# Kernel optimization log

Measured on AMD Instinct MI355X. Metric: run time of the kernel, lower is better.

## Reference

```python
import jax, jax.numpy as jnp
from jax import lax
import numpy as np

PRE_NMS_TOPN = 2000
POST_NMS_TOPN = 300
NMS_IOU_THRESHOLD = 0.7
EPS = 1e-8


def setup_inputs() -> dict:
    key = jax.random.key(0)
    k1, k2 = jax.random.split(key, 2)
    B, H, W, A = 64, 100, 100, 9
    # small-magnitude deltas so exp(dh/dw) stays sane, as real RPN outputs do
    rpn_bbox_deltas = jax.random.normal(k1, (B, H, W, A * 4), dtype=jnp.float32) * 0.1
    rpn_labels = jax.random.uniform(k2, (B, H, W, A), dtype=jnp.float32)
    # grid anchors, normalized coords, 3 scales x 3 ratios = 9 per position
    ys = (jnp.arange(H, dtype=jnp.float32) + 0.5) / H
    xs = (jnp.arange(W, dtype=jnp.float32) + 0.5) / W
    scales = jnp.array([0.1, 0.2, 0.4], dtype=jnp.float32)
    ratios = jnp.array([0.5, 1.0, 2.0], dtype=jnp.float32)
    hh = (scales[:, None] * jnp.sqrt(ratios)[None, :]).reshape(-1)  # [9]
    ww = (scales[:, None] / jnp.sqrt(ratios)[None, :]).reshape(-1)  # [9]
    cy, cx = jnp.meshgrid(ys, xs, indexing="ij")  # [H,W]
    cy, cx = cy[..., None], cx[..., None]         # [H,W,1]
    anchors = jnp.stack(
        [cy - hh / 2, cx - ww / 2, cy + hh / 2, cx + ww / 2], axis=-1
    ).reshape(-1, 4)  # [H*W*9, 4] = [90000, 4]
    return {"rpn_bbox_deltas": rpn_bbox_deltas, "rpn_labels": rpn_labels, "anchors": anchors}


def _decode_deltas(anchors, deltas):
    # anchors [N,4] (y1,x1,y2,x2), deltas [B,N,4] (dy,dx,dh,dw)
    anc_h = anchors[:, 2] - anchors[:, 0]
    anc_w = anchors[:, 3] - anchors[:, 1]
    anc_cy = anchors[:, 0] + 0.5 * anc_h
    anc_cx = anchors[:, 1] + 0.5 * anc_w
    h = jnp.exp(deltas[..., 2]) * anc_h
    w = jnp.exp(deltas[..., 3]) * anc_w
    cy = deltas[..., 0] * anc_h + anc_cy
    cx = deltas[..., 1] * anc_w + anc_cx
    y1 = cy - 0.5 * h
    x1 = cx - 0.5 * w
    return jnp.stack([y1, x1, y1 + h, x1 + w], axis=-1)  # [B,N,4]


def _nms_single(boxes):
    # boxes [PRE,4] already sorted by score descending; greedy hard NMS
    n = boxes.shape[0]
    area = jnp.maximum(boxes[:, 2] - boxes[:, 0], 0.0) * jnp.maximum(boxes[:, 3] - boxes[:, 1], 0.0)
    idx = jnp.arange(n)

    def body(i, keep):
        b = boxes[i]
        yy1 = jnp.maximum(b[0], boxes[:, 0])
        xx1 = jnp.maximum(b[1], boxes[:, 1])
        yy2 = jnp.minimum(b[2], boxes[:, 2])
        xx2 = jnp.minimum(b[3], boxes[:, 3])
        inter = jnp.maximum(yy2 - yy1, 0.0) * jnp.maximum(xx2 - xx1, 0.0)
        iou = inter / (area[i] + area - inter + EPS)
        suppress = (iou > NMS_IOU_THRESHOLD) & (idx > i) & keep[i]
        return keep & ~suppress

    keep = lax.fori_loop(0, n, body, jnp.ones((n,), dtype=bool))
    # compact kept boxes (score order) into fixed [POST,4], zero-padded
    pos = jnp.where(keep, jnp.cumsum(keep) - 1, POST_NMS_TOPN)
    pos = jnp.minimum(pos, POST_NMS_TOPN)
    out = jnp.zeros((POST_NMS_TOPN + 1, 4), dtype=boxes.dtype).at[pos].set(boxes)[:POST_NMS_TOPN]
    return jnp.clip(out, 0.0, 1.0)  # clip_boxes=True in tf combined NMS


def reference(rpn_bbox_deltas, rpn_labels, anchors):
    B = rpn_bbox_deltas.shape[0]
    N = anchors.shape[0]
    deltas = rpn_bbox_deltas.reshape(B, N, 4)
    labels = rpn_labels.reshape(B, N)
    boxes = _decode_deltas(anchors, deltas)             # [B,N,4]
    _, pre_idx = lax.top_k(labels, PRE_NMS_TOPN)        # [B,PRE] sorted desc
    pre_boxes = jnp.take_along_axis(boxes, pre_idx[..., None], axis=1)  # [B,PRE,4]
    roi_bboxes = jax.vmap(_nms_single)(pre_boxes)       # [B,POST,4]
    return lax.stop_gradient(roi_bboxes)
```

## Files before the change

### kernel.cpp

```cpp
#include <hip/hip_runtime.h>
#include <stdint.h>


#define PRE 2000
#define POST 300
#define TILE 512
#define IOU_THR 0.7f
#define EPSV 1e-8f
#define SORTN 2048
#define NBINS 2048
#define DESTCAP 4096
#define CANDCAP 512
#define CONS 1984
#define SL 16
#define KBUF 768

typedef unsigned long long u64;

__device__ __forceinline__ uint32_t flip_f32(uint32_t b) {
    return b ^ ((uint32_t)((int32_t)b >> 31) | 0x80000000u);
}

__device__ __forceinline__ int bin_of(float s) {
    int bn = (int)(s * 2048.0f);
    return min(max(bn, 0), NBINS - 1);
}

__device__ __forceinline__ u64 make_key(float s, int idx, int bn) {
    uint32_t ub = flip_f32(__float_as_uint(s));
    return ((u64)ub << 32) | ((uint32_t)bn << 20) |
           (uint32_t)(0xFFFFF - idx);
}

__device__ __forceinline__ bool iou_gt(const float4& bi, float ai,
                                       const float4& bj, float aj) {
    float yy1 = fmaxf(bi.x, bj.x);
    float xx1 = fmaxf(bi.y, bj.y);
    float yy2 = fminf(bi.z, bj.z);
    float xx2 = fminf(bi.w, bj.w);
    float inter = fmaxf(yy2 - yy1, 0.f) * fmaxf(xx2 - xx1, 0.f);
    float iou = inter / (ai + aj - inter + EPSV);
    return iou > IOU_THR;
}

__device__ __forceinline__ float area_of(const float4& bx) {
    return fmaxf(bx.z - bx.x, 0.f) * fmaxf(bx.w - bx.y, 0.f);
}

__device__ __forceinline__ float4 decode_key(u64 key, const float4* dl,
                                             const float4* anchors, int N) {
    uint32_t idx = 0xFFFFFu - (uint32_t)(key & 0xFFFFFull);
    if (idx >= (uint32_t)N) return make_float4(0.f, 0.f, 0.f, 0.f);
    float4 d  = dl[idx];
    float4 an = anchors[idx];
    float ah  = an.z - an.x;
    float aw  = an.w - an.y;
    float acy = an.x + 0.5f * ah;
    float acx = an.y + 0.5f * aw;
    float h   = expf(d.z) * ah;
    float w   = expf(d.w) * aw;
    float cy  = d.x * ah + acy;
    float cx  = d.y * aw + acx;
    float y1  = cy - 0.5f * h;
    float x1  = cx - 0.5f * w;
    return make_float4(y1, x1, y1 + h, x1 + w);
}

__device__ __forceinline__ u64 cs_keep(u64 v, u64 pv, int i, int j, int k) {
    bool lower   = ((i & j) == 0);
    bool desc    = ((i & k) == 0);
    bool keepmax = (desc == lower);
    u64 mx = v > pv ? v : pv;
    u64 mn = v > pv ? pv : v;
    return keepmax ? mx : mn;
}

__global__ __launch_bounds__(256) void k1_gather(
    const float4* __restrict__ score4,
    u64* __restrict__ g_pairs,
    int* __restrict__ g_scnt,
    uint32_t* __restrict__ g_shist,
    int N)
{
    const int blk = blockIdx.x;
    const int b   = blk / SL;
    const int s   = blk % SL;
    const int tid = threadIdx.x;
    const int lane = tid & 63;
    const int F4PB = N >> 2;
    const int F4PS = (F4PB + SL - 1) / SL;

    __shared__ u64 keybuf[KBUF];
    __shared__ u64 binbuf[KBUF];
    __shared__ uint32_t hist64[64];
    __shared__ int base64[64];
    __shared__ uint32_t cur64[64];
    __shared__ int kcnt;

    if (tid < 64) { hist64[tid] = 0u; cur64[tid] = 0u; }
    if (tid == 0) kcnt = 0;
    __syncthreads();

    const float4* src = score4 + (size_t)b * F4PB;
    const int n0 = s * F4PS, n1 = min(n0 + F4PS, F4PB);
    for (int n = n0 + tid; n < n1; n += 256) {
        float4 v = src[n];
        float sv[4] = {v.x, v.y, v.z, v.w};
#pragma unroll
        for (int c = 0; c < 4; ++c) {
            int bn = bin_of(sv[c]);
            if (bn >= CONS) {
                int q = atomicAdd(&kcnt, 1);
                if (q < KBUF) keybuf[q] = make_key(sv[c], 4 * n + c, bn);
            }
        }
    }
    __syncthreads();

    const int raw = kcnt;
    const int lc  = min(raw, KBUF);

    for (int i = tid; i < lc; i += 256) {
        int b64 = (int)((keybuf[i] >> 20) & 0xFFFu) - CONS;
        atomicAdd(&hist64[b64], 1u);
    }
    __syncthreads();

    if (tid < 64) {
        int h = (int)hist64[lane];
        int ssum = h;
#pragma unroll
        for (int off = 1; off < 64; off <<= 1) {
            int t = __shfl_down(ssum, off, 64);
            if (lane + off < 64) ssum += t;
        }
        base64[lane] = ssum - h;
    }
    __syncthreads();

    for (int i = tid; i < lc; i += 256) {
        u64 key = keybuf[i];
        int b64 = (int)((key >> 20) & 0xFFFu) - CONS;
        int p = (int)atomicAdd(&cur64[b64], 1u);
        binbuf[base64[b64] + p] = key;
    }
    __syncthreads();

    if (tid == 0) g_scnt[b * SL + s] = raw;
    if (tid < 64) g_shist[((size_t)b * SL + s) * 64 + tid] = hist64[tid];
    u64* gp = g_pairs + ((size_t)b * SL + s) * KBUF;
    for (int i = tid; i < lc; i += 256) gp[i] = binbuf[i];
}

__global__ __launch_bounds__(1024) void k2_sort(
    const float4* __restrict__ score4,
    const u64*  __restrict__ g_pairs,
    const int*  __restrict__ g_scnt,
    const uint32_t* __restrict__ g_shist,
    u64* __restrict__ g_sorted,
    int N)
{
    const int b    = blockIdx.x;
    const int tid  = threadIdx.x;
    const int lane = tid & 63;
    const int wv   = tid >> 6;

    __shared__ u64 dest[DESTCAP];
    __shared__ uint32_t hist2048[NBINS];
    __shared__ u64 cand[CANDCAP];
    __shared__ uint32_t shist[SL][64];
    __shared__ int srcb[SL][64];
    __shared__ int sbase[SL][64];
    __shared__ int tot64[64];
    __shared__ int segbase64[64];
    __shared__ uint32_t wtot[16];
    __shared__ int sh_flag, sh_total, sh_bsel, sh_tprime, sh_cnt, sh_nc;
    __shared__ uint32_t sh_pivot;

    const int F4PB = N >> 2;

    shist[tid >> 6][tid & 63] = g_shist[(size_t)b * SL * 64 + tid];
    if (tid == 0) {
        int f = 0;
#pragma unroll
        for (int s = 0; s < SL; ++s)
            if (g_scnt[b * SL + s] > KBUF) f = 1;
        sh_flag = f;
    }
    __syncthreads();

    if (tid < 64) {
        int acc = 0;
#pragma unroll
        for (int s = 0; s < SL; ++s) acc += (int)shist[s][tid];
        tot64[tid] = acc;
        if (acc > 128) sh_flag = 1;
    }
    {
        int h = (int)shist[wv][lane];
        int ssum = h;
#pragma unroll
        for (int off = 1; off < 64; off <<= 1) {
            int t = __shfl_down(ssum, off, 64);
            if (lane + off < 64) ssum += t;
        }
        srcb[wv][lane] = ssum - h;
    }
    __syncthreads();

    if (tid < 64) {
        int t0 = tot64[lane];
        int ssum = t0;
#pragma unroll
        for (int off = 1; off < 64; off <<= 1) {
            int t = __shfl_down(ssum, off, 64);
            if (lane + off < 64) ssum += t;
        }
        segbase64[lane] = ssum - t0;
        if (lane == 0) sh_total = ssum;
    }
    __syncthreads();
    const int total = sh_total;
    if (tid == 0 && (total < PRE || total > DESTCAP)) sh_flag = 1;
    {
        int s   = tid >> 6;
        int b64 = tid & 63;
        int pre = 0;
        for (int s2 = 0; s2 < s; ++s2) pre += (int)shist[s2][b64];
        sbase[s][b64] = segbase64[b64] + pre;
    }
    __syncthreads();
    const bool flag = (sh_flag != 0);

    if (!flag) {
        const int cs = min(g_scnt[b * SL + wv], KBUF);
        const u64* gp = g_pairs + ((size_t)b * SL + wv) * KBUF;
        for (int i = lane; i < cs; i += 64) {
            u64 key = gp[i];
            int b64 = (int)((key >> 20) & 0xFFFu) - CONS;
            dest[sbase[wv][b64] + (i - srcb[wv][b64])] = key;
        }
        __syncthreads();
        for (int sgi = wv; sgi < 64; sgi += 16) {
            int n = tot64[sgi];
            if (n <= 0) continue;
            int base = segbase64[sgi];
            if (n <= 64) {
                u64 e = (lane < n) ? dest[base + lane] : 0ull;
#pragma unroll
                for (int k = 2; k <= 64; k <<= 1)
                    for (int j = k >> 1; j > 0; j >>= 1)
                        e = cs_keep(e, __shfl_xor(e, j, 64), lane, j, k);
                if (lane < n) dest[base + lane] = e;
            } else {
                u64 e0 = (lane < n) ? dest[base + lane] : 0ull;
                u64 e1 = (lane + 64 < n) ? dest[base + lane + 64] : 0ull;
#pragma unroll
                for (int k = 2; k <= 128; k <<= 1) {
                    for (int j = k >> 1; j > 0; j >>= 1) {
                        if (j == 64) {
                            u64 a = e0, c = e1;
                            e0 = cs_keep(a, c, lane, 64, k);
                            e1 = cs_keep(c, a, lane + 64, 64, k);
                        } else {
                            e0 = cs_keep(e0, __shfl_xor(e0, j, 64), lane, j, k);
                            e1 = cs_keep(e1, __shfl_xor(e1, j, 64), lane + 64, j, k);
                        }
                    }
                }
                if (lane < n) dest[base + lane] = e0;
                if (lane + 64 < n) dest[base + lane + 64] = e1;
            }
        }
        __syncthreads();
        g_sorted[(size_t)b * SORTN + tid]        = dest[tid];
        g_sorted[(size_t)b * SORTN + tid + 1024] = dest[tid + 1024];
    } else {
        hist2048[tid] = 0u; hist2048[tid + 1024] = 0u;
        if (tid == 0) { sh_cnt = 0; sh_nc = 0; }
        __syncthreads();
        const float4* src = score4 + (size_t)b * F4PB;
        for (int n = tid; n < F4PB; n += 1024) {
            float4 v = src[n];
            atomicAdd(&hist2048[bin_of(v.x)], 1u);
            atomicAdd(&hist2048[bin_of(v.y)], 1u);
            atomicAdd(&hist2048[bin_of(v.z)], 1u);
            atomicAdd(&hist2048[bin_of(v.w)], 1u);
        }
        __syncthreads();
        {
            const int i0 = wv * 128 + lane;
            const int i1 = i0 + 64;
            int h0 = (int)hist2048[i0];
            int h1 = (int)hist2048[i1];
            int s0 = h0, s1 = h1;
#pragma unroll
            for (int off = 1; off < 64; off <<= 1) {
                int t0 = __shfl_down(s0, off, 64);
                int t1 = __shfl_down(s1, off, 64);
                if (lane + off < 64) { s0 += t0; s1 += t1; }
            }
            int sum_h1 = __shfl(s1, 0, 64);
            if (lane == 0) wtot[wv] = (uint32_t)(__shfl(s0, 0, 64) + sum_h1);
            __syncthreads();
            int offtot = 0;
            for (int w2 = wv + 1; w2 < 16; ++w2) offtot += (int)wtot[w2];
            int S0 = s0 + sum_h1 + offtot;
            int S1 = s1 + offtot;
            if (S0 >= PRE && S0 - h0 < PRE) { sh_bsel = i0; sh_tprime = PRE - (S0 - h0); }
            if (S1 >= PRE && S1 - h1 < PRE) { sh_bsel = i1; sh_tprime = PRE - (S1 - h1); }
        }
        __syncthreads();
        const int bsel   = sh_bsel;
        const int tprime = sh_tprime;
        for (int n = tid; n < F4PB; n += 1024) {
            float4 v = src[n];
            float sv[4] = {v.x, v.y, v.z, v.w};
#pragma unroll
            for (int c = 0; c < 4; ++c) {
                int bn = bin_of(sv[c]);
                if (bn >= bsel) {
                    u64 key = make_key(sv[c], 4 * n + c, bn);
                    if (bn > bsel) {
                        int q = atomicAdd(&sh_cnt, 1);
                        if (q < SORTN) dest[q] = key;
                    } else {
                        int t = atomicAdd(&sh_nc, 1);
                        if (t < CANDCAP) cand[t] = key;
                    }
                }
            }
        }
        __syncthreads();
        const int nc = min(sh_nc, CANDCAP);
        for (int i = tid; i < nc; i += 1024) {
            uint32_t vi = (uint32_t)(cand[i] >> 32);
            int g = 0, e = 0;
            for (int j = 0; j < nc; ++j) {
                uint32_t vj = (uint32_t)(cand[j] >> 32);
                g += (vj > vi);
                e += (vj == vi);
            }
            if (g < tprime && g + e >= tprime) sh_pivot = vi;
        }
        __syncthreads();
        const uint32_t pivot = sh_pivot;
        for (int i = tid; i < nc; i += 1024) {
            uint32_t vi = (uint32_t)(cand[i] >> 32);
            if (vi >= pivot) {
                int q = atomicAdd(&sh_cnt, 1);
                if (q < SORTN) dest[q] = cand[i];
            }
        }
        __syncthreads();
        const int tt = min(sh_cnt, SORTN);
        for (int q = tt + tid; q < SORTN; q += 1024) dest[q] = 0ull;
        __syncthreads();
        {
            const int i0 = wv * 128 + lane;
            const int i1 = i0 + 64;
            u64 e0 = dest[i0];
            u64 e1 = dest[i1];
            for (int k = 2; k <= SORTN; k <<= 1) {
                for (int j = k >> 1; j > 0; j >>= 1) {
                    if (j >= 128) {
                        dest[i0] = e0;
                        dest[i1] = e1;
                        __syncthreads();
                        u64 p0 = dest[i0 ^ j];
                        u64 p1 = dest[i1 ^ j];
                        __syncthreads();
                        e0 = cs_keep(e0, p0, i0, j, k);
                        e1 = cs_keep(e1, p1, i1, j, k);
                    } else if (j == 64) {
                        u64 a = e0, c = e1;
                        e0 = cs_keep(a, c, i0, 64, k);
                        e1 = cs_keep(c, a, i1, 64, k);
                    } else {
                        e0 = cs_keep(e0, __shfl_xor(e0, j, 64), i0, j, k);
                        e1 = cs_keep(e1, __shfl_xor(e1, j, 64), i1, j, k);
                    }
                }
            }
            g_sorted[(size_t)b * SORTN + i0] = e0;
            g_sorted[(size_t)b * SORTN + i1] = e1;
        }
    }
}

__global__ __launch_bounds__(256) void k4_supmat(
    const float4* __restrict__ deltas,
    const float4* __restrict__ anchors,
    const u64*  __restrict__ g_sorted,
    float4* __restrict__ g_boxes,
    uint32_t* __restrict__ g_supmat,
    uint32_t* __restrict__ g_supT,
    int N)
{
    const int b   = blockIdx.x >> 4;
    const int s   = blockIdx.x & 15;
    const int tid = threadIdx.x;

    __shared__ float4 box[TILE];

    const float4* dl = deltas + (size_t)b * N;
#pragma unroll
    for (int k = 0; k < 2; ++k) {
        int r = tid + k * 256;
        box[r] = decode_key(g_sorted[(size_t)b * SORTN + r], dl, anchors, N);
    }
    __syncthreads();

    if (s == 0) {
#pragma unroll
        for (int k = 0; k < 2; ++k) {
            int r = tid + k * 256;
            g_boxes[(size_t)b * TILE + r] = box[r];
        }
    }

    const int rbase = s * 32;
#pragma unroll
    for (int k = 0; k < 2; ++k) {
        int idx = tid + k * 256;
        int row = rbase + (idx & 31);
        int w   = idx >> 5;
        int jbase = w << 5;
        float4 bi = box[row];
        float  ai = area_of(bi);
        uint32_t bits = 0u;
        if (jbase + 31 > row) {
#pragma unroll
            for (int c = 0; c < 32; ++c) {
                int j = jbase + c;
                float4 bj = box[j];
                float  aj = area_of(bj);
                bool gt = (j > row) & iou_gt(bi, ai, bj, aj);
                bits |= ((uint32_t)gt) << c;
            }
        }
        g_supmat[((size_t)b * TILE + row) * 16 + w] = bits;
    }

    if (s < 8 && tid < 128) {
        int q  = s;
        int j  = tid >> 1;
        int w2 = tid & 1;
        int C  = q * 64 + j;
        float4 bc = box[C];
        float  ac = area_of(bc);
        uint32_t bits = 0u;
#pragma unroll
        for (int c = 0; c < 32; ++c) {
            int R = q * 64 + w2 * 32 + c;
            float4 br = box[R];
            float  ar = area_of(br);
            bool gt = (R < C) & iou_gt(br, ar, bc, ac);
            bits |= ((uint32_t)gt) << c;
        }
        g_supT[((size_t)b * TILE + C) * 2 + w2] = bits;
    }
}

__global__ __launch_bounds__(64) void k5_sweep(
    const uint32_t* __restrict__ g_supmat,
    const u64*    __restrict__ g_supT64,
    const u64*    __restrict__ g_sorted,
    const float4* __restrict__ deltas,
    const float4* __restrict__ anchors,
    const float4* __restrict__ g_boxes,
    float4* __restrict__ out,
    int N)
{
    const int b    = blockIdx.x;
    const int lane = threadIdx.x;

    __shared__ uint32_t kept[POST];
    __shared__ u64 sh_keepbits[TILE / 64];
    __shared__ int sh_kc;
    __shared__ float4 fbox[PRE];
    __shared__ float  farea[PRE];
    __shared__ uint32_t fmask[(PRE - TILE + 31) / 32];

    const u64* tdbase = g_supT64 + (size_t)b * TILE;

    uint32_t removedw = 0u;
    int kc = 0, nq = 0;
    u64 cw_cur = tdbase[lane];
    for (int q = 0; q < TILE / 64; ++q) {
        u64 cw_next = (q < TILE / 64 - 1) ? tdbase[(q + 1) * 64 + lane] : 0ull;
        const int cbase = q << 6;
        uint32_t rlo = (uint32_t)__builtin_amdgcn_readlane((int)removedw, 2 * q);
        uint32_t rhi = (uint32_t)__builtin_amdgcn_readlane((int)removedw, 2 * q + 1);
        u64 avail = ~(((u64)rhi << 32) | rlo);
        u64 K = 0ull;
        while (avail) {
            int i = __ffsll((long long)avail) - 1;
            K |= (1ull << i);
            u64 supp = __ballot(((cw_cur >> i) & 1ull) != 0ull);
            avail &= ~(supp | (1ull << i));
        }
        if (lane == 0) sh_keepbits[q] = K;
        kc += __popcll(K);
        nq = q + 1;
        if (kc >= POST) break;
        if (K) {
            const int w = lane & 15;
            const int g = lane >> 4;
            const uint32_t* gs =
                g_supmat + ((size_t)b * TILE + cbase + g * 16) * 16 + w;
            uint32_t acc = 0u;
#pragma unroll
            for (int r = 0; r < 16; ++r) {
                uint32_t v = gs[(size_t)r * 16];
                uint32_t m = (uint32_t)0 - (uint32_t)((K >> (g * 16 + r)) & 1ull);
                acc |= (v & m);
            }
            acc |= (uint32_t)__shfl_xor((int)acc, 16, 64);
            acc |= (uint32_t)__shfl_xor((int)acc, 32, 64);
            if (lane < 16) removedw |= acc;
        }
        cw_cur = cw_next;
    }
    {
        int base = 0;
        for (int q = 0; q < nq; ++q) {
            u64 kbq = sh_keepbits[q];
            int pos = base + __popcll(kbq & ((1ull << lane) - 1));
            if (((kbq >> lane) & 1ull) && pos < POST)
                kept[pos] = (uint32_t)(q * 64 + lane);
            base += __popcll(kbq);
        }
        if (lane == 0) sh_kc = min(kc, POST);
    }
    __syncthreads();
    int kcf = sh_kc;
    const bool fellback = (kcf < POST);

    if (fellback) {
        const float4* dl = deltas + (size_t)b * N;
        for (int r = lane; r < PRE; r += 64) {
            float4 bx = decode_key(g_sorted[(size_t)b * SORTN + r], dl,
                                   anchors, N);
            fbox[r]  = bx;
            farea[r] = area_of(bx);
        }
        for (int w = lane; w < (PRE - TILE + 31) / 32; w += 64) fmask[w] = 0u;
        __syncthreads();
        for (int j = TILE + lane; j < PRE; j += 64) {
            float4 bj = fbox[j];
            float  aj = farea[j];
            bool supd = false;
            for (int k = 0; k < kcf; ++k) {
                int i = (int)kept[k];
                if (iou_gt(fbox[i], farea[i], bj, aj)) { supd = true; break; }
            }
            if (supd) atomicOr(&fmask[(j - TILE) >> 5], 1u << ((j - TILE) & 31));
        }
        __syncthreads();
        int i = TILE;
        while (i < PRE && kcf < POST) {
            while (i < PRE && ((fmask[(i - TILE) >> 5] >> ((i - TILE) & 31)) & 1u)) ++i;
            if (i >= PRE) break;
            if (lane == 0) kept[kcf] = (uint32_t)i;
            ++kcf;
            if (kcf >= POST) break;
            float4 bi = fbox[i];
            float  ai = farea[i];
            for (int j = i + 1 + lane; j < PRE; j += 64) {
                if (iou_gt(bi, ai, fbox[j], farea[j]))
                    atomicOr(&fmask[(j - TILE) >> 5], 1u << ((j - TILE) & 31));
            }
            ++i;
            __syncthreads();
        }
    }
    __syncthreads();

    float4* ob = out + (size_t)b * POST;
    for (int r = lane; r < POST; r += 64) {
        float4 o = make_float4(0.f, 0.f, 0.f, 0.f);
        if (r < kcf) {
            int ki = (int)kept[r];
            float4 bx = fellback ? fbox[ki]
                                 : g_boxes[(size_t)b * TILE + ki];
            o.x = fminf(fmaxf(bx.x, 0.f), 1.f);
            o.y = fminf(fmaxf(bx.y, 0.f), 1.f);
            o.z = fminf(fmaxf(bx.z, 0.f), 1.f);
            o.w = fminf(fmaxf(bx.w, 0.f), 1.f);
        }
        ob[r] = o;
    }
}

extern "C" void kernel_launch(void* const* d_in, const int* in_sizes, int n_in,
                              void* d_out, int out_size, void* d_ws, size_t ws_size,
                              hipStream_t stream) {
    const float4* deltas  = (const float4*)d_in[0];
    const float*  labels  = (const float*)d_in[1];
    const float4* anchors = (const float4*)d_in[2];
    const float4* score4  = (const float4*)labels;
    float4*       outp    = (float4*)d_out;
    const int N = in_sizes[2] / 4;
    const int B = in_sizes[1] / N;

    char* ws = (char*)d_ws;
    const size_t SZ_BOXES  = (size_t)B * TILE * 16;
    const size_t SZ_PAIRS  = (size_t)B * SL * KBUF * 8;
    const size_t SZ_SORTED = (size_t)B * SORTN * 8;
    const size_t SZ_SUPMAT = (size_t)B * TILE * 16 * 4;
    const size_t SZ_SUPT   = (size_t)B * TILE * 8;
    const size_t SZ_SHIST  = (size_t)B * SL * 64 * 4;
    float4*   g_boxes  = (float4*)ws;
    u64*      g_pairs  = (u64*)(ws + SZ_BOXES);
    u64*      g_sorted = (u64*)(ws + SZ_BOXES + SZ_PAIRS);
    uint32_t* g_supmat = (uint32_t*)(ws + SZ_BOXES + SZ_PAIRS + SZ_SORTED);
    uint32_t* g_supT   = (uint32_t*)(ws + SZ_BOXES + SZ_PAIRS + SZ_SORTED + SZ_SUPMAT);
    uint32_t* g_shist  = (uint32_t*)(ws + SZ_BOXES + SZ_PAIRS + SZ_SORTED + SZ_SUPMAT + SZ_SUPT);
    int*      g_scnt   = (int*)((char*)g_shist + SZ_SHIST);

    k1_gather<<<B * SL, 256, 0, stream>>>(score4, g_pairs, g_scnt, g_shist, N);
    k2_sort<<<B, 1024, 0, stream>>>(score4, g_pairs, g_scnt, g_shist,
                                    g_sorted, N);
    k4_supmat<<<B * 16, 256, 0, stream>>>(deltas, anchors, g_sorted,
                                          g_boxes, g_supmat, g_supT, N);
    k5_sweep<<<B, 64, 0, stream>>>(g_supmat, (const u64*)g_supT, g_sorted,
                                   deltas, anchors, g_boxes, outp, N);
}
```

Measured before the change: 75.68 us.

## Fuse four NMS pipeline kernels into one cooperative mega-kernel with grid syncs

Replaces the four separate launches (gather, sort, suppression matrix, sweep) with one cooperative kernel that runs each phase in turn, separated by grid-wide syncs, and shares a union of LDS layouts. This removes launch gaps and the drain between kernels. The sort phase is reworked for 256-thread blocks: the slice count is halved with a larger per-slice buffer, the prefix-scan offsets are recomputed, and the fallback bitonic sort runs as strided loops. A fallback path keeps four 256-thread kernels for when the cooperative launch cannot fit. The risks are the cost of grid.sync, the narrower sort phase (1024 threads down to 256), and host-side occupancy queries made on every call.

After: 101.5 us. 34.1% more time.

```diff
diff --git a/kernel.cpp b/kernel.cpp
--- a/kernel.cpp
+++ b/kernel.cpp
@@ -1,4 +1,5 @@
 #include <hip/hip_runtime.h>
+#include <hip/hip_cooperative_groups.h>
 #include <stdint.h>
 
 
@@ -9,13 +10,14 @@
 #define EPSV 1e-8f
 #define SORTN 2048
 #define NBINS 2048
-#define DESTCAP 4096
+#define DESTCAP 3584
 #define CANDCAP 512
 #define CONS 1984
-#define SL 16
-#define KBUF 768
+#define SL 8
+#define KBUF 1536
 
 typedef unsigned long long u64;
+namespace cg = cooperative_groups;
 
 __device__ __forceinline__ uint32_t flip_f32(uint32_t b) {
     return b ^ ((uint32_t)((int32_t)b >> 31) | 0x80000000u);
@@ -75,30 +77,43 @@
     return keepmax ? mx : mn;
 }
 
-__global__ __launch_bounds__(256) void k1_gather(
-    const float4* __restrict__ score4,
-    u64* __restrict__ g_pairs,
-    int* __restrict__ g_scnt,
-    uint32_t* __restrict__ g_shist,
-    int N)
-{
-    const int blk = blockIdx.x;
-    const int b   = blk / SL;
-    const int s   = blk % SL;
-    const int tid = threadIdx.x;
+struct P1L {
+    u64 keybuf[KBUF];
+    u64 binbuf[KBUF];
+    uint32_t hist64[64];
+    int base64[64];
+    uint32_t cur64[64];
+    int kcnt;
+};
+struct P2L {
+    u64 dest[DESTCAP];
+    int off[SL][64];
+    int tot64[64];
+    int segbase64[64];
+    int flag, total, bsel, tprime, cnt, nc;
+    uint32_t pivot;
+};
+struct P3L { float4 box[TILE]; };
+struct P4L {
+    uint32_t kept[POST];
+    u64 keepbits[TILE / 64];
+    uint32_t fmask[(PRE - TILE + 31) / 32];
+};
+union MegaLDS { P1L p1; P2L p2; P3L p3; P4L p4; };
+
+__device__ void phase1(MegaLDS& u, int blk, int tid,
+                       const float4* __restrict__ score4,
+                       u64* __restrict__ g_pairs, int* __restrict__ g_scnt,
+                       uint32_t* __restrict__ g_shist, int N)
+{
+    const int b = blk / SL;
+    const int s = blk % SL;
     const int lane = tid & 63;
     const int F4PB = N >> 2;
     const int F4PS = (F4PB + SL - 1) / SL;
 
-    __shared__ u64 keybuf[KBUF];
-    __shared__ u64 binbuf[KBUF];
-    __shared__ uint32_t hist64[64];
-    __shared__ int base64[64];
-    __shared__ uint32_t cur64[64];
-    __shared__ int kcnt;
-
-    if (tid < 64) { hist64[tid] = 0u; cur64[tid] = 0u; }
-    if (tid == 0) kcnt = 0;
+    if (tid < 64) { u.p1.hist64[tid] = 0u; u.p1.cur64[tid] = 0u; }
+    if (tid == 0) u.p1.kcnt = 0;
     __syncthreads();
 
     const float4* src = score4 + (size_t)b * F4PB;
@@ -110,151 +125,127 @@
         for (int c = 0; c < 4; ++c) {
             int bn = bin_of(sv[c]);
             if (bn >= CONS) {
-                int q = atomicAdd(&kcnt, 1);
-                if (q < KBUF) keybuf[q] = make_key(sv[c], 4 * n + c, bn);
-            }
-        }
-    }
-    __syncthreads();
-
-    const int raw = kcnt;
+                int q = atomicAdd(&u.p1.kcnt, 1);
+                if (q < KBUF) u.p1.keybuf[q] = make_key(sv[c], 4 * n + c, bn);
+            }
+        }
+    }
+    __syncthreads();
+
+    const int raw = u.p1.kcnt;
     const int lc  = min(raw, KBUF);
 
     for (int i = tid; i < lc; i += 256) {
-        int b64 = (int)((keybuf[i] >> 20) & 0xFFFu) - CONS;
-        atomicAdd(&hist64[b64], 1u);
+        int b64 = (int)((u.p1.keybuf[i] >> 20) & 0xFFFu) - CONS;
+        atomicAdd(&u.p1.hist64[b64], 1u);
     }
     __syncthreads();
 
     if (tid < 64) {
-        int h = (int)hist64[lane];
+        int h = (int)u.p1.hist64[lane];
         int ssum = h;
 #pragma unroll
         for (int off = 1; off < 64; off <<= 1) {
             int t = __shfl_down(ssum, off, 64);
             if (lane + off < 64) ssum += t;
         }
-        base64[lane] = ssum - h;
+        u.p1.base64[lane] = ssum - h;
     }
     __syncthreads();
 
     for (int i = tid; i < lc; i += 256) {
-        u64 key = keybuf[i];
+        u64 key = u.p1.keybuf[i];
         int b64 = (int)((key >> 20) & 0xFFFu) - CONS;
-        int p = (int)atomicAdd(&cur64[b64], 1u);
-        binbuf[base64[b64] + p] = key;
+        int p = (int)atomicAdd(&u.p1.cur64[b64], 1u);
+        u.p1.binbuf[u.p1.base64[b64] + p] = key;
     }
     __syncthreads();
 
     if (tid == 0) g_scnt[b * SL + s] = raw;
-    if (tid < 64) g_shist[((size_t)b * SL + s) * 64 + tid] = hist64[tid];
+    if (tid < 64) g_shist[((size_t)b * SL + s) * 64 + tid] = u.p1.hist64[tid];
     u64* gp = g_pairs + ((size_t)b * SL + s) * KBUF;
-    for (int i = tid; i < lc; i += 256) gp[i] = binbuf[i];
-}
-
-__global__ __launch_bounds__(1024) void k2_sort(
-    const float4* __restrict__ score4,
-    const u64*  __restrict__ g_pairs,
-    const int*  __restrict__ g_scnt,
-    const uint32_t* __restrict__ g_shist,
-    u64* __restrict__ g_sorted,
-    int N)
-{
-    const int b    = blockIdx.x;
-    const int tid  = threadIdx.x;
+    for (int i = tid; i < lc; i += 256) gp[i] = u.p1.binbuf[i];
+}
+
+__device__ void phase2(MegaLDS& u, int b, int tid,
+                       const float4* __restrict__ score4,
+                       const u64* __restrict__ g_pairs,
+                       const int* __restrict__ g_scnt,
+                       const uint32_t* __restrict__ g_shist,
+                       u64* __restrict__ g_sorted, int N)
+{
     const int lane = tid & 63;
-    const int wv   = tid >> 6;
-
-    __shared__ u64 dest[DESTCAP];
-    __shared__ uint32_t hist2048[NBINS];
-    __shared__ u64 cand[CANDCAP];
-    __shared__ uint32_t shist[SL][64];
-    __shared__ int srcb[SL][64];
-    __shared__ int sbase[SL][64];
-    __shared__ int tot64[64];
-    __shared__ int segbase64[64];
-    __shared__ uint32_t wtot[16];
-    __shared__ int sh_flag, sh_total, sh_bsel, sh_tprime, sh_cnt, sh_nc;
-    __shared__ uint32_t sh_pivot;
-
+    const int wv4  = tid >> 6;
     const int F4PB = N >> 2;
 
-    shist[tid >> 6][tid & 63] = g_shist[(size_t)b * SL * 64 + tid];
+    uint32_t* sh = (uint32_t*)u.p2.dest;
+    for (int i = tid; i < SL * 64; i += 256)
+        sh[i] = g_shist[(size_t)b * SL * 64 + i];
     if (tid == 0) {
         int f = 0;
-#pragma unroll
         for (int s = 0; s < SL; ++s)
             if (g_scnt[b * SL + s] > KBUF) f = 1;
-        sh_flag = f;
+        u.p2.flag = f;
     }
     __syncthreads();
 
     if (tid < 64) {
         int acc = 0;
 #pragma unroll
-        for (int s = 0; s < SL; ++s) acc += (int)shist[s][tid];
-        tot64[tid] = acc;
-        if (acc > 128) sh_flag = 1;
-    }
-    {
-        int h = (int)shist[wv][lane];
-        int ssum = h;
+        for (int s = 0; s < SL; ++s) acc += (int)sh[s * 64 + tid];
+        u.p2.tot64[tid] = acc;
+        if (acc > 128) u.p2.flag = 1;
+        int ssum = acc;
 #pragma unroll
         for (int off = 1; off < 64; off <<= 1) {
             int t = __shfl_down(ssum, off, 64);
             if (lane + off < 64) ssum += t;
         }
-        srcb[wv][lane] = ssum - h;
-    }
-    __syncthreads();
-
-    if (tid < 64) {
-        int t0 = tot64[lane];
-        int ssum = t0;
-#pragma unroll
-        for (int off = 1; off < 64; off <<= 1) {
-            int t = __shfl_down(ssum, off, 64);
-            if (lane + off < 64) ssum += t;
-        }
-        segbase64[lane] = ssum - t0;
-        if (lane == 0) sh_total = ssum;
-    }
-    __syncthreads();
-    const int total = sh_total;
-    if (tid == 0 && (total < PRE || total > DESTCAP)) sh_flag = 1;
-    {
-        int s   = tid >> 6;
-        int b64 = tid & 63;
+        u.p2.segbase64[tid] = ssum - acc;
+        if (tid == 0) u.p2.total = ssum;
+    }
+    __syncthreads();
+    const int total = u.p2.total;
+    if (tid == 0 && (total < PRE || total > DESTCAP)) u.p2.flag = 1;
+    for (int e = tid; e < SL * 64; e += 256) {
+        int s = e >> 6, b64 = e & 63;
         int pre = 0;
-        for (int s2 = 0; s2 < s; ++s2) pre += (int)shist[s2][b64];
-        sbase[s][b64] = segbase64[b64] + pre;
-    }
-    __syncthreads();
-    const bool flag = (sh_flag != 0);
+        for (int s2 = 0; s2 < s; ++s2) pre += (int)sh[s2 * 64 + b64];
+        int srcb = 0;
+        for (int b2 = b64 + 1; b2 < 64; ++b2) srcb += (int)sh[s * 64 + b2];
+        u.p2.off[s][b64] = u.p2.segbase64[b64] + pre - srcb;
+    }
+    __syncthreads();
+    const bool flag = (u.p2.flag != 0);
 
     if (!flag) {
-        const int cs = min(g_scnt[b * SL + wv], KBUF);
-        const u64* gp = g_pairs + ((size_t)b * SL + wv) * KBUF;
-        for (int i = lane; i < cs; i += 64) {
-            u64 key = gp[i];
-            int b64 = (int)((key >> 20) & 0xFFFu) - CONS;
-            dest[sbase[wv][b64] + (i - srcb[wv][b64])] = key;
-        }
-        __syncthreads();
-        for (int sgi = wv; sgi < 64; sgi += 16) {
-            int n = tot64[sgi];
+#pragma unroll
+        for (int si = 0; si < 2; ++si) {
+            int s = wv4 * 2 + si;
+            const int cs = min(g_scnt[b * SL + s], KBUF);
+            const u64* gp = g_pairs + ((size_t)b * SL + s) * KBUF;
+            for (int i = lane; i < cs; i += 64) {
+                u64 key = gp[i];
+                int b64 = (int)((key >> 20) & 0xFFFu) - CONS;
+                u.p2.dest[u.p2.off[s][b64] + i] = key;
+            }
+        }
+        for (int q = total + tid; q < SORTN; q += 256) u.p2.dest[q] = 0ull;
+        __syncthreads();
+        for (int sgi = wv4; sgi < 64; sgi += 4) {
+            int n = u.p2.tot64[sgi];
             if (n <= 0) continue;
-            int base = segbase64[sgi];
+            int base = u.p2.segbase64[sgi];
             if (n <= 64) {
-                u64 e = (lane < n) ? dest[base + lane] : 0ull;
+                u64 e = (lane < n) ? u.p2.dest[base + lane] : 0ull;
 #pragma unroll
                 for (int k = 2; k <= 64; k <<= 1)
                     for (int j = k >> 1; j > 0; j >>= 1)
                         e = cs_keep(e, __shfl_xor(e, j, 64), lane, j, k);
-                if (lane < n) dest[base + lane] = e;
+                if (lane < n) u.p2.dest[base + lane] = e;
             } else {
-                u64 e0 = (lane < n) ? dest[base + lane] : 0ull;
-                u64 e1 = (lane + 64 < n) ? dest[base + lane + 64] : 0ull;
+                u64 e0 = (lane < n) ? u.p2.dest[base + lane] : 0ull;
+                u64 e1 = (lane + 64 < n) ? u.p2.dest[base + lane + 64] : 0ull;
 #pragma unroll
                 for (int k = 2; k <= 128; k <<= 1) {
                     for (int j = k >> 1; j > 0; j >>= 1) {
@@ -268,19 +259,21 @@
                         }
                     }
                 }
-                if (lane < n) dest[base + lane] = e0;
-                if (lane + 64 < n) dest[base + lane + 64] = e1;
-            }
-        }
-        __syncthreads();
-        g_sorted[(size_t)b * SORTN + tid]        = dest[tid];
-        g_sorted[(size_t)b * SORTN + tid + 1024] = dest[tid + 1024];
+                if (lane < n) u.p2.dest[base + lane] = e0;
+                if (lane + 64 < n) u.p2.dest[base + lane + 64] = e1;
+            }
+        }
+        __syncthreads();
+        for (int r = tid; r < SORTN; r += 256)
+            g_sorted[(size_t)b * SORTN + r] = u.p2.dest[r];
     } else {
-        hist2048[tid] = 0u; hist2048[tid + 1024] = 0u;
-        if (tid == 0) { sh_cnt = 0; sh_nc = 0; }
+        uint32_t* hist2048 = (uint32_t*)&u.p2.dest[2048];
+        u64*      cand     = &u.p2.dest[3072];
+        for (int i = tid; i < NBINS; i += 256) hist2048[i] = 0u;
+        if (tid == 0) { u.p2.cnt = 0; u.p2.nc = 0; }
         __syncthreads();
         const float4* src = score4 + (size_t)b * F4PB;
-        for (int n = tid; n < F4PB; n += 1024) {
+        for (int n = tid; n < F4PB; n += 256) {
             float4 v = src[n];
             atomicAdd(&hist2048[bin_of(v.x)], 1u);
             atomicAdd(&hist2048[bin_of(v.y)], 1u);
@@ -288,32 +281,29 @@
             atomicAdd(&hist2048[bin_of(v.w)], 1u);
         }
         __syncthreads();
-        {
-            const int i0 = wv * 128 + lane;
-            const int i1 = i0 + 64;
-            int h0 = (int)hist2048[i0];
-            int h1 = (int)hist2048[i1];
-            int s0 = h0, s1 = h1;
-#pragma unroll
-            for (int off = 1; off < 64; off <<= 1) {
-                int t0 = __shfl_down(s0, off, 64);
-                int t1 = __shfl_down(s1, off, 64);
-                if (lane + off < 64) { s0 += t0; s1 += t1; }
-            }
-            int sum_h1 = __shfl(s1, 0, 64);
-            if (lane == 0) wtot[wv] = (uint32_t)(__shfl(s0, 0, 64) + sum_h1);
-            __syncthreads();
-            int offtot = 0;
-            for (int w2 = wv + 1; w2 < 16; ++w2) offtot += (int)wtot[w2];
-            int S0 = s0 + sum_h1 + offtot;
-            int S1 = s1 + offtot;
-            if (S0 >= PRE && S0 - h0 < PRE) { sh_bsel = i0; sh_tprime = PRE - (S0 - h0); }
-            if (S1 >= PRE && S1 - h1 < PRE) { sh_bsel = i1; sh_tprime = PRE - (S1 - h1); }
-        }
-        __syncthreads();
-        const int bsel   = sh_bsel;
-        const int tprime = sh_tprime;
-        for (int n = tid; n < F4PB; n += 1024) {
+        if (tid < 64) {
+            int carry = 0;
+            for (int c = 31; c >= 0; --c) {
+                int h = (int)hist2048[c * 64 + lane];
+                int s = h;
+#pragma unroll
+                for (int off = 1; off < 64; off <<= 1) {
+                    int t = __shfl_down(s, off, 64);
+                    if (lane + off < 64) s += t;
+                }
+                int S = s + carry;
+                int Snext = S - h;
+                if (S >= PRE && Snext < PRE) {
+                    u.p2.bsel   = c * 64 + lane;
+                    u.p2.tprime = PRE - Snext;
+                }
+                carry += __shfl(s, 0, 64);
+            }
+        }
+        __syncthreads();
+        const int bsel   = u.p2.bsel;
+        const int tprime = u.p2.tprime;
+        for (int n = tid; n < F4PB; n += 256) {
             float4 v = src[n];
             float sv[4] = {v.x, v.y, v.z, v.w};
 #pragma unroll
@@ -322,18 +312,18 @@
                 if (bn >= bsel) {
                     u64 key = make_key(sv[c], 4 * n + c, bn);
                     if (bn > bsel) {
-                        int q = atomicAdd(&sh_cnt, 1);
-                        if (q < SORTN) dest[q] = key;
+                        int q = atomicAdd(&u.p2.cnt, 1);
+                        if (q < 2048) u.p2.dest[q] = key;
                     } else {
-                        int t = atomicAdd(&sh_nc, 1);
+                        int t = atomicAdd(&u.p2.nc, 1);
                         if (t < CANDCAP) cand[t] = key;
                     }
                 }
             }
         }
         __syncthreads();
-        const int nc = min(sh_nc, CANDCAP);
-        for (int i = tid; i < nc; i += 1024) {
+        const int nc = min(u.p2.nc, CANDCAP);
+        for (int i = tid; i < nc; i += 256) {
             uint32_t vi = (uint32_t)(cand[i] >> 32);
             int g = 0, e = 0;
             for (int j = 0; j < nc; ++j) {
@@ -341,73 +331,56 @@
                 g += (vj > vi);
                 e += (vj == vi);
             }
-            if (g < tprime && g + e >= tprime) sh_pivot = vi;
-        }
-        __syncthreads();
-        const uint32_t pivot = sh_pivot;
-        for (int i = tid; i < nc; i += 1024) {
+            if (g < tprime && g + e >= tprime) u.p2.pivot = vi;
+        }
+        __syncthreads();
+        const uint32_t pivot = u.p2.pivot;
+        for (int i = tid; i < nc; i += 256) {
             uint32_t vi = (uint32_t)(cand[i] >> 32);
             if (vi >= pivot) {
-                int q = atomicAdd(&sh_cnt, 1);
-                if (q < SORTN) dest[q] = cand[i];
-            }
-        }
-        __syncthreads();
-        const int tt = min(sh_cnt, SORTN);
-        for (int q = tt + tid; q < SORTN; q += 1024) dest[q] = 0ull;
-        __syncthreads();
-        {
-            const int i0 = wv * 128 + lane;
-            const int i1 = i0 + 64;
-            u64 e0 = dest[i0];
-            u64 e1 = dest[i1];
-            for (int k = 2; k <= SORTN; k <<= 1) {
-                for (int j = k >> 1; j > 0; j >>= 1) {
-                    if (j >= 128) {
-                        dest[i0] = e0;
-                        dest[i1] = e1;
-                        __syncthreads();
-                        u64 p0 = dest[i0 ^ j];
-                        u64 p1 = dest[i1 ^ j];
-                        __syncthreads();
-                        e0 = cs_keep(e0, p0, i0, j, k);
-                        e1 = cs_keep(e1, p1, i1, j, k);
-                    } else if (j == 64) {
-                        u64 a = e0, c = e1;
-                        e0 = cs_keep(a, c, i0, 64, k);
-                        e1 = cs_keep(c, a, i1, 64, k);
-                    } else {
-                        e0 = cs_keep(e0, __shfl_xor(e0, j, 64), i0, j, k);
-                        e1 = cs_keep(e1, __shfl_xor(e1, j, 64), i1, j, k);
-                    }
+                int q = atomicAdd(&u.p2.cnt, 1);
+                if (q < 2048) u.p2.dest[q] = cand[i];
+            }
+        }
+        __syncthreads();
+        const int tt = min(u.p2.cnt, 2048);
+        for (int q = tt + tid; q < SORTN; q += 256) u.p2.dest[q] = 0ull;
+        __syncthreads();
+        for (int k = 2; k <= SORTN; k <<= 1) {
+            for (int j = k >> 1; j > 0; j >>= 1) {
+                for (int p = tid; p < SORTN / 2; p += 256) {
+                    int i = 2 * p - (p & (j - 1));
+                    int l = i | j;
+                    u64 a = u.p2.dest[i], c = u.p2.dest[l];
+                    bool up = ((i & k) == 0);
+                    bool sw = up ? (a < c) : (a > c);
+                    if (sw) { u.p2.dest[i] = c; u.p2.dest[l] = a; }
                 }
-            }
-            g_sorted[(size_t)b * SORTN + i0] = e0;
-            g_sorted[(size_t)b * SORTN + i1] = e1;
-        }
-    }
-}
-
-__global__ __launch_bounds__(256) void k4_supmat(
-    const float4* __restrict__ deltas,
-    const float4* __restrict__ anchors,
-    const u64*  __restrict__ g_sorted,
-    float4* __restrict__ g_boxes,
-    uint32_t* __restrict__ g_supmat,
-    uint32_t* __restrict__ g_supT,
-    int N)
-{
-    const int b   = blockIdx.x >> 4;
-    const int s   = blockIdx.x & 15;
-    const int tid = threadIdx.x;
-
-    __shared__ float4 box[TILE];
+                __syncthreads();
+            }
+        }
+        for (int r = tid; r < SORTN; r += 256)
+            g_sorted[(size_t)b * SORTN + r] = u.p2.dest[r];
+    }
+}
+
+__device__ void phase3(MegaLDS& u, int blk, int tid,
+                       const float4* __restrict__ deltas,
+                       const float4* __restrict__ anchors,
+                       const u64* __restrict__ g_sorted,
+                       float4* __restrict__ g_boxes,
+                       uint32_t* __restrict__ g_supmat,
+                       uint32_t* __restrict__ g_supT, int N)
+{
+    const int b = blk >> 3;
+    const int s = blk & 7;
 
     const float4* dl = deltas + (size_t)b * N;
 #pragma unroll
     for (int k = 0; k < 2; ++k) {
         int r = tid + k * 256;
-        box[r] = decode_key(g_sorted[(size_t)b * SORTN + r], dl, anchors, N);
+        u.p3.box[r] = decode_key(g_sorted[(size_t)b * SORTN + r], dl,
+                                 anchors, N);
     }
     __syncthreads();
 
@@ -415,25 +388,25 @@
 #pragma unroll
         for (int k = 0; k < 2; ++k) {
             int r = tid + k * 256;
-            g_boxes[(size_t)b * TILE + r] = box[r];
-        }
-    }
-
-    const int rbase = s * 32;
-#pragma unroll
-    for (int k = 0; k < 2; ++k) {
+            g_boxes[(size_t)b * TILE + r] = u.p3.box[r];
+        }
+    }
+
+    const int rbase = s * 64;
+#pragma unroll
+    for (int k = 0; k < 4; ++k) {
         int idx = tid + k * 256;
-        int row = rbase + (idx & 31);
-        int w   = idx >> 5;
+        int row = rbase + (idx & 63);
+        int w   = idx >> 6;
         int jbase = w << 5;
-        float4 bi = box[row];
+        float4 bi = u.p3.box[row];
         float  ai = area_of(bi);
         uint32_t bits = 0u;
         if (jbase + 31 > row) {
 #pragma unroll
             for (int c = 0; c < 32; ++c) {
                 int j = jbase + c;
-                float4 bj = box[j];
+                float4 bj = u.p3.box[j];
                 float  aj = area_of(bj);
                 bool gt = (j > row) & iou_gt(bi, ai, bj, aj);
                 bits |= ((uint32_t)gt) << c;
@@ -442,18 +415,18 @@
         g_supmat[((size_t)b * TILE + row) * 16 + w] = bits;
     }
 
-    if (s < 8 && tid < 128) {
+    if (tid < 128) {
         int q  = s;
         int j  = tid >> 1;
         int w2 = tid & 1;
         int C  = q * 64 + j;
-        float4 bc = box[C];
+        float4 bc = u.p3.box[C];
         float  ac = area_of(bc);
         uint32_t bits = 0u;
 #pragma unroll
         for (int c = 0; c < 32; ++c) {
             int R = q * 64 + w2 * 32 + c;
-            float4 br = box[R];
+            float4 br = u.p3.box[R];
             float  ar = area_of(br);
             bool gt = (R < C) & iou_gt(br, ar, bc, ac);
             bits |= ((uint32_t)gt) << c;
@@ -462,26 +435,16 @@
     }
 }
 
-__global__ __launch_bounds__(64) void k5_sweep(
-    const uint32_t* __restrict__ g_supmat,
-    const u64*    __restrict__ g_supT64,
-    const u64*    __restrict__ g_sorted,
-    const float4* __restrict__ deltas,
-    const float4* __restrict__ anchors,
-    const float4* __restrict__ g_boxes,
-    float4* __restrict__ out,
-    int N)
-{
-    const int b    = blockIdx.x;
-    const int lane = threadIdx.x;
-
-    __shared__ uint32_t kept[POST];
-    __shared__ u64 sh_keepbits[TILE / 64];
-    __shared__ int sh_kc;
-    __shared__ float4 fbox[PRE];
-    __shared__ float  farea[PRE];
-    __shared__ uint32_t fmask[(PRE - TILE + 31) / 32];
-
+__device__ void phase4(MegaLDS& u, int b, int lane,
+                       const uint32_t* __restrict__ g_supmat,
+                       const u64* __restrict__ g_supT64,
+                       const u64* __restrict__ g_sorted,
+                       const float4* __restrict__ deltas,
+                       const float4* __restrict__ anchors,
+                       const float4* __restrict__ g_boxes,
+                       float4* __restrict__ fb,
+                       float4* __restrict__ out, int N)
+{
     const u64* tdbase = g_supT64 + (size_t)b * TILE;
 
     uint32_t removedw = 0u;
@@ -500,7 +463,7 @@
             u64 supp = __ballot(((cw_cur >> i) & 1ull) != 0ull);
             avail &= ~(supp | (1ull << i));
         }
-        if (lane == 0) sh_keepbits[q] = K;
+        if (lane == 0) u.p4.keepbits[q] = K;
         kc += __popcll(K);
         nq = q + 1;
         if (kc >= POST) break;
@@ -525,65 +488,60 @@
     {
         int base = 0;
         for (int q = 0; q < nq; ++q) {
-            u64 kbq = sh_keepbits[q];
+            u64 kbq = u.p4.keepbits[q];
             int pos = base + __popcll(kbq & ((1ull << lane) - 1));
             if (((kbq >> lane) & 1ull) && pos < POST)
-                kept[pos] = (uint32_t)(q * 64 + lane);
+                u.p4.kept[pos] = (uint32_t)(q * 64 + lane);
             base += __popcll(kbq);
         }
-        if (lane == 0) sh_kc = min(kc, POST);
-    }
-    __syncthreads();
-    int kcf = sh_kc;
+    }
+    int kcf = min(kc, POST);
     const bool fellback = (kcf < POST);
 
     if (fellback) {
         const float4* dl = deltas + (size_t)b * N;
-        for (int r = lane; r < PRE; r += 64) {
-            float4 bx = decode_key(g_sorted[(size_t)b * SORTN + r], dl,
-                                   anchors, N);
-            fbox[r]  = bx;
-            farea[r] = area_of(bx);
-        }
-        for (int w = lane; w < (PRE - TILE + 31) / 32; w += 64) fmask[w] = 0u;
-        __syncthreads();
+        for (int r = lane; r < PRE; r += 64)
+            fb[r] = decode_key(g_sorted[(size_t)b * SORTN + r], dl, anchors, N);
+        for (int w = lane; w < (PRE - TILE + 31) / 32; w += 64)
+            u.p4.fmask[w] = 0u;
         for (int j = TILE + lane; j < PRE; j += 64) {
-            float4 bj = fbox[j];
-            float  aj = farea[j];
+            float4 bj = fb[j];
+            float  aj = area_of(bj);
             bool supd = false;
             for (int k = 0; k < kcf; ++k) {
-                int i = (int)kept[k];
-                if (iou_gt(fbox[i], farea[i], bj, aj)) { supd = true; break; }
-            }
-            if (supd) atomicOr(&fmask[(j - TILE) >> 5], 1u << ((j - TILE) & 31));
-        }
-        __syncthreads();
+                int i = (int)u.p4.kept[k];
+                float4 bi = fb[i];
+                if (iou_gt(bi, area_of(bi), bj, aj)) { supd = true; break; }
+            }
+            if (supd)
+                atomicOr(&u.p4.fmask[(j - TILE) >> 5], 1u << ((j - TILE) & 31));
+        }
         int i = TILE;
         while (i < PRE && kcf < POST) {
-            while (i < PRE && ((fmask[(i - TILE) >> 5] >> ((i - TILE) & 31)) & 1u)) ++i;
+            while (i < PRE &&
+                   ((u.p4.fmask[(i - TILE) >> 5] >> ((i - TILE) & 31)) & 1u)) ++i;
             if (i >= PRE) break;
-            if (lane == 0) kept[kcf] = (uint32_t)i;
+            if (lane == 0) u.p4.kept[kcf] = (uint32_t)i;
             ++kcf;
             if (kcf >= POST) break;
-            float4 bi = fbox[i];
-            float  ai = farea[i];
+            float4 bi = fb[i];
+            float  ai = area_of(bi);
             for (int j = i + 1 + lane; j < PRE; j += 64) {
-                if (iou_gt(bi, ai, fbox[j], farea[j]))
-                    atomicOr(&fmask[(j - TILE) >> 5], 1u << ((j - TILE) & 31));
+                float4 bj = fb[j];
+                if (iou_gt(bi, ai, bj, area_of(bj)))
+                    atomicOr(&u.p4.fmask[(j - TILE) >> 5],
+                             1u << ((j - TILE) & 31));
             }
             ++i;
-            __syncthreads();
-        }
-    }
-    __syncthreads();
+        }
+    }
 
     float4* ob = out + (size_t)b * POST;
     for (int r = lane; r < POST; r += 64) {
         float4 o = make_float4(0.f, 0.f, 0.f, 0.f);
         if (r < kcf) {
-            int ki = (int)kept[r];
-            float4 bx = fellback ? fbox[ki]
-                                 : g_boxes[(size_t)b * TILE + ki];
+            int ki = (int)u.p4.kept[r];
+            float4 bx = fellback ? fb[ki] : g_boxes[(size_t)b * TILE + ki];
             o.x = fminf(fmaxf(bx.x, 0.f), 1.f);
             o.y = fminf(fmaxf(bx.y, 0.f), 1.f);
             o.z = fminf(fmaxf(bx.z, 0.f), 1.f);
@@ -591,6 +549,78 @@
         }
         ob[r] = o;
     }
+}
+
+__global__ __launch_bounds__(256, 2) void mega_kernel(
+    const float4* __restrict__ score4,
+    const float4* __restrict__ deltas,
+    const float4* __restrict__ anchors,
+    u64*      __restrict__ g_pairs,
+    int*      __restrict__ g_scnt,
+    uint32_t* __restrict__ g_shist,
+    u64*      __restrict__ g_sorted,
+    float4*   __restrict__ g_boxes,
+    uint32_t* __restrict__ g_supmat,
+    uint32_t* __restrict__ g_supT,
+    float4*   __restrict__ fb_scratch,
+    float4*   __restrict__ out,
+    int N, int B)
+{
+    cg::grid_group grid = cg::this_grid();
+    const int blk = blockIdx.x;
+    const int tid = threadIdx.x;
+    __shared__ MegaLDS u;
+
+    phase1(u, blk, tid, score4, g_pairs, g_scnt, g_shist, N);
+    grid.sync();
+    if (blk < B)
+        phase2(u, blk, tid, score4, g_pairs, g_scnt, g_shist, g_sorted, N);
+    grid.sync();
+    phase3(u, blk, tid, deltas, anchors, g_sorted, g_boxes, g_supmat,
+           g_supT, N);
+    grid.sync();
+    if (blk < B && tid < 64)
+        phase4(u, blk, tid, g_supmat, (const u64*)g_supT, g_sorted, deltas,
+               anchors, g_boxes, fb_scratch + (size_t)blk * PRE, out, N);
+}
+
+__global__ __launch_bounds__(256) void k_p1(
+    const float4* __restrict__ score4, u64* __restrict__ g_pairs,
+    int* __restrict__ g_scnt, uint32_t* __restrict__ g_shist, int N)
+{
+    __shared__ MegaLDS u;
+    phase1(u, blockIdx.x, threadIdx.x, score4, g_pairs, g_scnt, g_shist, N);
+}
+
+__global__ __launch_bounds__(256) void k_p2(
+    const float4* __restrict__ score4, const u64* __restrict__ g_pairs,
+    const int* __restrict__ g_scnt, const uint32_t* __restrict__ g_shist,
+    u64* __restrict__ g_sorted, int N)
+{
+    __shared__ MegaLDS u;
+    phase2(u, blockIdx.x, threadIdx.x, score4, g_pairs, g_scnt, g_shist,
+           g_sorted, N);
+}
+
+__global__ __launch_bounds__(256) void k_p3(
+    const float4* __restrict__ deltas, const float4* __restrict__ anchors,
+    const u64* __restrict__ g_sorted, float4* __restrict__ g_boxes,
+    uint32_t* __restrict__ g_supmat, uint32_t* __restrict__ g_supT, int N)
+{
+    __shared__ MegaLDS u;
+    phase3(u, blockIdx.x, threadIdx.x, deltas, anchors, g_sorted, g_boxes,
+           g_supmat, g_supT, N);
+}
+
+__global__ __launch_bounds__(64) void k_p4(
+    const uint32_t* __restrict__ g_supmat, const u64* __restrict__ g_supT64,
+    const u64* __restrict__ g_sorted, const float4* __restrict__ deltas,
+    const float4* __restrict__ anchors, const float4* __restrict__ g_boxes,
+    float4* __restrict__ fb_scratch, float4* __restrict__ out, int N)
+{
+    __shared__ MegaLDS u;
+    phase4(u, blockIdx.x, threadIdx.x, g_supmat, g_supT64, g_sorted, deltas,
+           anchors, g_boxes, fb_scratch + (size_t)blockIdx.x * PRE, out, N);
 }
 
 extern "C" void kernel_launch(void* const* d_in, const int* in_sizes, int n_in,
@@ -601,8 +631,8 @@
     const float4* anchors = (const float4*)d_in[2];
     const float4* score4  = (const float4*)labels;
     float4*       outp    = (float4*)d_out;
-    const int N = in_sizes[2] / 4;
-    const int B = in_sizes[1] / N;
+    int N = in_sizes[2] / 4;
+    int B = in_sizes[1] / N;
 
     char* ws = (char*)d_ws;
     const size_t SZ_BOXES  = (size_t)B * TILE * 16;
@@ -618,12 +648,30 @@
     uint32_t* g_supT   = (uint32_t*)(ws + SZ_BOXES + SZ_PAIRS + SZ_SORTED + SZ_SUPMAT);
     uint32_t* g_shist  = (uint32_t*)(ws + SZ_BOXES + SZ_PAIRS + SZ_SORTED + SZ_SUPMAT + SZ_SUPT);
     int*      g_scnt   = (int*)((char*)g_shist + SZ_SHIST);
-
-    k1_gather<<<B * SL, 256, 0, stream>>>(score4, g_pairs, g_scnt, g_shist, N);
-    k2_sort<<<B, 1024, 0, stream>>>(score4, g_pairs, g_scnt, g_shist,
-                                    g_sorted, N);
-    k4_supmat<<<B * 16, 256, 0, stream>>>(deltas, anchors, g_sorted,
-                                          g_boxes, g_supmat, g_supT, N);
-    k5_sweep<<<B, 64, 0, stream>>>(g_supmat, (const u64*)g_supT, g_sorted,
-                                   deltas, anchors, g_boxes, outp, N);
-}
+    float4*   fb       = (float4*)g_pairs;
+
+    int dev = 0, numCU = 0, maxB = 0;
+    hipGetDevice(&dev);
+    hipDeviceGetAttribute(&numCU, hipDeviceAttributeMultiprocessorCount, dev);
+    hipOccupancyMaxActiveBlocksPerMultiprocessor(&maxB, (const void*)mega_kernel,
+                                                 256, 0);
+    const int grid = B * SL;
+    if ((long long)maxB * numCU >= grid) {
+        void* args[] = {
+            (void*)&score4, (void*)&deltas, (void*)&anchors,
+            (void*)&g_pairs, (void*)&g_scnt, (void*)&g_shist,
+            (void*)&g_sorted, (void*)&g_boxes, (void*)&g_supmat,
+            (void*)&g_supT, (void*)&fb, (void*)&outp, (void*)&N, (void*)&B
+        };
+        hipError_t e = hipLaunchCooperativeKernel((void*)mega_kernel,
+                                                  dim3(grid), dim3(256),
+                                                  args, 0, stream);
+        if (e == hipSuccess) return;
+    }
+    k_p1<<<B * SL, 256, 0, stream>>>(score4, g_pairs, g_scnt, g_shist, N);
+    k_p2<<<B, 256, 0, stream>>>(score4, g_pairs, g_scnt, g_shist, g_sorted, N);
+    k_p3<<<B * SL, 256, 0, stream>>>(deltas, anchors, g_sorted, g_boxes,
+                                     g_supmat, g_supT, N);
+    k_p4<<<B, 64, 0, stream>>>(g_supmat, (const u64*)g_supT, g_sorted,
+                               deltas, anchors, g_boxes, fb, outp, N);
+}
```
